# Optimization experiments

Hardware: AMD Instinct MI355X
Metric: run time of the kernel (lower is better)

## Reference

```python
import jax, jax.numpy as jnp
import numpy as np

B, L, C, D, H, NB, K = 8, 1024, 4, 64, 8, 2, 16  # batch, seq, conds, dim, heads, blocks, rbf centers

def _ln(x, s, b):
    m = x.mean(-1, keepdims=True)
    v = x.var(-1, keepdims=True)
    return (x - m) / jnp.sqrt(v + 1e-6) * s + b

def setup_inputs() -> dict:
    key = jax.random.key(0)
    ks = jax.random.split(key, 24)
    rn = lambda i, shape, sc=0.02: jax.random.normal(ks[i], shape, jnp.float32) * sc
    inp = {}
    inp['z'] = jax.random.normal(ks[0], (B, L), jnp.float32)
    inp['conditionals'] = jax.random.normal(ks[1], (C,), jnp.float32)
    inp['s'] = jnp.sort(jax.random.uniform(ks[2], (L,), jnp.float32))
    inp['embed'] = rn(3, (L, 2 * D - (C + 1)))  # positional id embedding table
    # input MLP([4D, D]) with gelu
    inp['Win1'] = rn(4, (2 * D, 4 * D)); inp['bin1'] = jnp.zeros((4 * D,), jnp.float32)
    inp['Win2'] = rn(5, (4 * D, D));     inp['bin2'] = jnp.zeros((D,), jnp.float32)
    # per-block (leading dim NB) transformer params
    inp['ln1_s'] = jnp.ones((NB, D), jnp.float32); inp['ln1_b'] = jnp.zeros((NB, D), jnp.float32)
    inp['ln2_s'] = jnp.ones((NB, D), jnp.float32); inp['ln2_b'] = jnp.zeros((NB, D), jnp.float32)
    inp['Wq'] = rn(6, (NB, D, 2 * D)); inp['bq'] = jnp.zeros((NB, 2 * D), jnp.float32)
    inp['Wk'] = rn(7, (NB, D, 2 * D)); inp['bk'] = jnp.zeros((NB, 2 * D), jnp.float32)
    inp['Wv'] = rn(8, (NB, D, 2 * D)); inp['bv'] = jnp.zeros((NB, 2 * D), jnp.float32)
    inp['Wo'] = rn(9, (NB, 2 * D, D)); inp['bo'] = jnp.zeros((NB, D), jnp.float32)
    # RBF-network attention bias: features exp(-(d-c)^2/(2w^2)) -> linear to H heads
    inp['rbf_c'] = jnp.tile(jnp.linspace(-1.0, 1.0, K, dtype=jnp.float32)[None], (NB, 1))
    inp['rbf_logw'] = jnp.full((NB, K), -1.0, jnp.float32)
    inp['rbf_w'] = rn(10, (NB, K, H), 0.1); inp['rbf_b'] = jnp.zeros((NB, H), jnp.float32)
    # FFN MLP([4D, D])
    inp['W1'] = rn(11, (NB, D, 4 * D)); inp['b1'] = jnp.zeros((NB, 4 * D), jnp.float32)
    inp['W2'] = rn(12, (NB, 4 * D, D)); inp['b2'] = jnp.zeros((NB, D), jnp.float32)
    # head MLP([4D, D, 1])
    inp['Wh1'] = rn(13, (D, 4 * D)); inp['bh1'] = jnp.zeros((4 * D,), jnp.float32)
    inp['Wh2'] = rn(14, (4 * D, D)); inp['bh2'] = jnp.zeros((D,), jnp.float32)
    inp['Wh3'] = rn(15, (D, 1));     inp['bh3'] = jnp.zeros((1,), jnp.float32)
    return inp

def reference(z, conditionals, s, embed, Win1, bin1, Win2, bin2,
              ln1_s, ln1_b, ln2_s, ln2_b, Wq, bq, Wk, bk, Wv, bv, Wo, bo,
              rbf_c, rbf_logw, rbf_w, rbf_b, W1, b1, W2, b2,
              Wh1, bh1, Wh2, bh2, Wh3, bh3):
    Bn, Ln = z.shape
    Cn = conditionals.shape[0]
    Hn = rbf_w.shape[-1]
    dh = Wq.shape[-1] // Hn
    scale = 1.0 / jnp.sqrt(jnp.float32(dh))
    # cond_as_feats: [z, broadcast conditionals] -> (B, L, C+1); prepend ids embedding -> (B, L, 2D)
    feats = jnp.concatenate([
        jnp.broadcast_to(embed[None], (Bn,) + embed.shape),
        z[..., None],
        jnp.broadcast_to(conditionals[None, None, :], (Bn, Ln, Cn)),
    ], axis=-1)
    x = jax.nn.gelu(feats @ Win1 + bin1) @ Win2 + bin2  # (B, L, D)
    dist = s[:, None] - s[None, :]  # (L, L) pairwise query-key coordinate diff (same per batch)
    for i in range(Wq.shape[0]):
        h = _ln(x, ln1_s[i], ln1_b[i])
        q = (h @ Wq[i] + bq[i]).reshape(Bn, Ln, Hn, dh)
        k = (h @ Wk[i] + bk[i]).reshape(Bn, Ln, Hn, dh)
        v = (h @ Wv[i] + bv[i]).reshape(Bn, Ln, Hn, dh)
        scores = jnp.einsum('bqhd,bkhd->bhqk', q, k) * scale
        # RBF-network bias on pairwise distances, per head
        phi = jnp.exp(-(dist[..., None] - rbf_c[i]) ** 2 / (2.0 * jnp.exp(rbf_logw[i]) ** 2))  # (L, L, K)
        bias = jnp.einsum('qkf,fh->hqk', phi, rbf_w[i]) + rbf_b[i][:, None, None]  # (H, L, L)
        a = jax.nn.softmax(scores + bias[None], axis=-1)
        o = jnp.einsum('bhqk,bkhd->bqhd', a, v).reshape(Bn, Ln, Hn * dh)
        x = x + o @ Wo[i] + bo[i]
        h2 = _ln(x, ln2_s[i], ln2_b[i])
        x = x + jax.nn.gelu(h2 @ W1[i] + b1[i]) @ W2[i] + b2[i]
    hh = jax.nn.gelu(x @ Wh1 + bh1)
    hh = jax.nn.gelu(hh @ Wh2 + bh2)
    return hh @ Wh3 + bh3  # f_hat: (B, L, 1)
```

## Files before the change

### kernel.cpp

```cpp
#include <hip/hip_runtime.h>
#include <hip/hip_bf16.h>

#define BB   8
#define LL   1024
#define DD   64
#define D2   128
#define D4   256
#define HH   8
#define DH   16

typedef __attribute__((ext_vector_type(8))) short short8;
typedef __attribute__((ext_vector_type(4))) float floatx4;

#define LOG2E 1.4426950408889634f
#define QK_SEED -66.54214054f

#define OFF_WIN1   0
#define OFF_WIN2   65536
#define OFF_LAY0   98304
#define LAY_STRIDE 131072
#define OFF_WQ     0
#define OFF_WK     16384
#define OFF_WV     32768
#define OFF_WO     49152
#define OFF_W1     65536
#define OFF_W2     98304
#define OFF_WH1    360448
#define OFF_WH2    393216

__device__ __forceinline__ float gelu_tanh(float u) {
  float t = tanhf(0.7978845608028654f * (u + 0.044715f * u * u * u));
  return 0.5f * u * (1.0f + t);
}

__device__ __forceinline__ float wave_reduce_sum(float v) {
#pragma unroll
  for (int m = 32; m >= 1; m >>= 1) v += __shfl_xor(v, m, 64);
  return v;
}

__device__ __forceinline__ unsigned short f2bf(float x) {
  unsigned u = __float_as_uint(x);
  u += 0x7fffu + ((u >> 16) & 1u);
  return (unsigned short)(u >> 16);
}

__device__ __forceinline__ float bf2f(unsigned short x) {
  return __uint_as_float(((unsigned)x) << 16);
}

__device__ __forceinline__ void split_bf(float v, unsigned short& hi,
                                         unsigned short& lo) {
  hi = f2bf(v);
  lo = f2bf(v - bf2f(hi));
}

__device__ __forceinline__ unsigned pack_bf2(float a, float b) {
  unsigned ua = __float_as_uint(a) + 0x8000u;
  unsigned ub = __float_as_uint(b) + 0x8000u;
  return __builtin_amdgcn_perm(ub, ua, 0x07060302u);
}

template <int K, int KP>
__device__ __forceinline__ floatx4 mfma_tile(
    const unsigned short* Ah, const unsigned short* Al,
    const unsigned short* __restrict__ Bh, const unsigned short* __restrict__ Bl,
    int lq, int quad, floatx4 C) {
#pragma unroll
  for (int kk = 0; kk < K; kk += 32) {
    short8 ah = *(const short8*)(Ah + lq * KP + kk + quad * 8);
    short8 al = *(const short8*)(Al + lq * KP + kk + quad * 8);
    short8 bh = *(const short8*)(Bh + lq * K + kk + quad * 8);
    short8 bl = *(const short8*)(Bl + lq * K + kk + quad * 8);
    C = __builtin_amdgcn_mfma_f32_16x16x32_bf16(ah, bh, C, 0, 0, 0);
    C = __builtin_amdgcn_mfma_f32_16x16x32_bf16(al, bh, C, 0, 0, 0);
    C = __builtin_amdgcn_mfma_f32_16x16x32_bf16(ah, bl, C, 0, 0, 0);
  }
  return C;
}

struct PrepArgs {
  const float* src[16];
  int Kd[16], Nd[16], dst[16], elems[16];
};

__global__ __launch_bounds__(256) void k_prep_bias(
    PrepArgs a, unsigned short* __restrict__ arena,
    const float* __restrict__ s, const float* __restrict__ rbf_c,
    const float* __restrict__ rbf_logw, const float* __restrict__ rbf_w,
    const float* __restrict__ rbf_b, unsigned short* __restrict__ biasT) {
  int bid = blockIdx.x, t = threadIdx.x;
  if (bid < 2048) {
    int mid = bid >> 7;
    int e = (bid & 127) * 256 + t;
    int KN = a.elems[mid];
    if (e >= KN) return;
    int K = a.Kd[mid], N = a.Nd[mid];
    int n = e / K, k = e - n * K;
    float wv = a.src[mid][k * N + n];
    unsigned short hi, lo;
    split_bf(wv, hi, lo);
    arena[a.dst[mid] + e] = hi;
    arena[a.dst[mid] + KN + e] = lo;
    return;
  }
  int rem = bid - 2048;
  int lay = rem >> 12;
  int id = (rem & 4095) * 256 + t;
  int q = id >> 10, k = id & 1023;
  float dd = s[q] - s[k];
  float acc[8];
#pragma unroll
  for (int h = 0; h < 8; ++h) acc[h] = rbf_b[lay * 8 + h];
#pragma unroll 1
  for (int f = 0; f < 16; ++f) {
    float c = rbf_c[lay * 16 + f];
    float inv2w2 = 0.5f * __expf(-2.0f * rbf_logw[lay * 16 + f]);
    float e = dd - c;
    float ph = __expf(-e * e * inv2w2);
#pragma unroll
    for (int h = 0; h < 8; ++h)
      acc[h] = fmaf(ph, rbf_w[lay * 128 + f * 8 + h], acc[h]);
  }
  unsigned short* bT = biasT + (size_t)lay * 8 * 1024 * 1024;
#pragma unroll
  for (int h = 0; h < 8; ++h)
    bT[(size_t)(h * 1024 + q) * 1024 + k] = f2bf(acc[h] * LOG2E);
}

__device__ __forceinline__ void qkv_tail(
    const float* xl, unsigned short* Sh, unsigned short* Sl,
    const unsigned short* __restrict__ arena, int lay,
    const float* __restrict__ ln_s, const float* __restrict__ ln_b,
    const float* __restrict__ bq, const float* __restrict__ bk,
    const float* __restrict__ bv, unsigned short* __restrict__ qo,
    unsigned short* __restrict__ ko, unsigned short* __restrict__ voT,
    int tok0, int t) {
  int w = t >> 6, lane = t & 63;
  int lq = lane & 15, quad = lane >> 4;
  float ss = ln_s[lay * 64 + lane], sb = ln_b[lay * 64 + lane];
#pragma unroll
  for (int tk = 0; tk < 4; ++tk) {
    int tok = w * 4 + tk;
    float v = xl[tok * 64 + lane];
    float mean = wave_reduce_sum(v) * 0.015625f;
    float d = v - mean;
    float var = wave_reduce_sum(d * d) * 0.015625f;
    float hv = d * rsqrtf(var + 1e-6f) * ss + sb;
    unsigned short hi, lo;
    split_bf(hv, hi, lo);
    Sh[tok * 72 + lane] = hi;
    Sl[tok * 72 + lane] = lo;
  }
  __syncthreads();
  int b = tok0 >> 10, l0 = tok0 & 1023;
#pragma unroll 1
  for (int mat = 0; mat < 3; ++mat) {
    const unsigned short* Bh =
        arena + OFF_LAY0 + lay * LAY_STRIDE + mat * 16384;
    const unsigned short* Bl = Bh + 8192;
    const float* bias = (mat == 0 ? bq : mat == 1 ? bk : bv) + lay * 128;
#pragma unroll
    for (int j = 0; j < 2; ++j) {
      int tl = w + j * 4;
      int n = tl * 16 + lq;
      float bb = bias[n];
      floatx4 C = {bb, bb, bb, bb};
      C = mfma_tile<64, 72>(Sh, Sl, Bh + tl * 16 * 64, Bl + tl * 16 * 64,
                            lq, quad, C);
      if (mat < 2) {
        unsigned short* outp = (mat == 0 ? qo : ko);
        size_t basea = ((size_t)(b * 8 + tl) * 1024 + l0 + quad * 4) * 16 + lq;
#pragma unroll
        for (int r = 0; r < 4; ++r)
          outp[basea + (size_t)r * 16] = f2bf(C[r]);
      } else {
        size_t basev = ((size_t)(b * 8 + tl) * 16 + lq) * 1024 + l0 + quad * 4;
#pragma unroll
        for (int r = 0; r < 4; ++r)
          voT[basev + r] = f2bf(C[r]);
      }
    }
  }
}

__global__ __launch_bounds__(256) void k_in_qkv(
    const float* __restrict__ embed, const float* __restrict__ z,
    const float* __restrict__ cond, const unsigned short* __restrict__ arena,
    const float* __restrict__ bin1, const float* __restrict__ bin2,
    float* __restrict__ x, const float* __restrict__ ln1_s,
    const float* __restrict__ ln1_b, const float* __restrict__ bq,
    const float* __restrict__ bk, const float* __restrict__ bv,
    unsigned short* __restrict__ qo, unsigned short* __restrict__ ko,
    unsigned short* __restrict__ voT) {
  __shared__ __align__(16) unsigned short Ah[16 * 136], Al[16 * 136];
  __shared__ __align__(16) unsigned short Hh[16 * 264], Hl[16 * 264];
  __shared__ __align__(16) unsigned short Sh[16 * 72], Sl[16 * 72];
  __shared__ float xl[16 * 64];
  int t = threadIdx.x, w = t >> 6, lane = t & 63;
  int lq = lane & 15, quad = lane >> 4;
  int tok0 = blockIdx.x * 16;
  for (int idx = t; idx < 2048; idx += 256) {
    int tok = idx >> 7, dim = idx & 127;
    int bl = tok0 + tok, l = bl & (LL - 1);
    float v;
    if (dim < 123) v = embed[l * 123 + dim];
    else if (dim == 123) v = z[bl];
    else v = cond[dim - 124];
    unsigned short hi, lo;
    split_bf(v, hi, lo);
    Ah[tok * 136 + dim] = hi;
    Al[tok * 136 + dim] = lo;
  }
  __syncthreads();
  const unsigned short* B1h = arena + OFF_WIN1;
  const unsigned short* B1l = B1h + 32768;
#pragma unroll
  for (int j = 0; j < 4; ++j) {
    int tl = w * 4 + j, n = tl * 16 + lq;
    float bb = bin1[n];
    floatx4 C = {bb, bb, bb, bb};
    C = mfma_tile<128, 136>(Ah, Al, B1h + tl * 16 * 128, B1l + tl * 16 * 128,
                            lq, quad, C);
#pragma unroll
    for (int r = 0; r < 4; ++r) {
      float g = gelu_tanh(C[r]);
      unsigned short hi, lo;
      split_bf(g, hi, lo);
      Hh[(quad * 4 + r) * 264 + n] = hi;
      Hl[(quad * 4 + r) * 264 + n] = lo;
    }
  }
  __syncthreads();
  const unsigned short* B2h = arena + OFF_WIN2;
  const unsigned short* B2l = B2h + 16384;
  {
    int n = w * 16 + lq;
    float bb = bin2[n];
    floatx4 C = {bb, bb, bb, bb};
    C = mfma_tile<256, 264>(Hh, Hl, B2h + w * 16 * 256, B2l + w * 16 * 256,
                            lq, quad, C);
#pragma unroll
    for (int r = 0; r < 4; ++r) {
      int m = quad * 4 + r;
      x[(size_t)(tok0 + m) * 64 + n] = C[r];
      xl[m * 64 + n] = C[r];
    }
  }
  __syncthreads();
  qkv_tail(xl, Sh, Sl, arena, 0, ln1_s, ln1_b, bq, bk, bv,
           qo, ko, voT, tok0, t);
}

__global__ __launch_bounds__(256) void k_attn(
    const unsigned short* __restrict__ qg, const unsigned short* __restrict__ kg,
    const unsigned short* __restrict__ vgT, const unsigned short* __restrict__ biasT,
    float* __restrict__ og) {
  __shared__ __align__(16) unsigned short Kl[64 * 32];
  __shared__ __align__(16) unsigned short VT[16 * 72];
  __shared__ __align__(16) unsigned short Pl[4][16 * 72];
  __shared__ __align__(16) unsigned short Bch[64 * 72];
  int t = threadIdx.x, w = t >> 6, lane = t & 63;
  int lq = lane & 15, quad = lane >> 4;
  int bid = blockIdx.x;
  int b = bid >> 7, h = (bid >> 4) & 7, qblk = bid & 15;
  int q0w = qblk * 64 + w * 16;
  size_t bh = (size_t)(b * 8 + h) * 1024;
  size_t bh16 = (size_t)(b * 8 + h) * 16;

  ((uint4*)Kl)[t] = uint4{0, 0, 0, 0};

  short8 Qb = {};
  if (quad < 2)
    Qb = *(const short8*)(qg + (bh + q0w + lq) * 16 + quad * 8);

  float l = 0.0f;
  floatx4 O = {0.0f, 0.0f, 0.0f, 0.0f};

  int key = t >> 2, dp = (t & 3) * 4;
  int drow = t >> 4, vcol = (t & 15) * 4;
  int qrow = t >> 2, bcol = (t & 3) * 16;
  const unsigned short* kgp = kg + (bh + key) * 16 + dp;
  const unsigned short* vgp = vgT + (bh16 + drow) * 1024 + vcol;
  const unsigned short* bgp =
      biasT + ((size_t)(h * 1024 + qblk * 64 + qrow)) * 1024 + bcol;

  uint2 kpre = *(const uint2*)(kgp);
  uint2 vpre = *(const uint2*)(vgp);
  uint4 bpre0 = *(const uint4*)(bgp);
  uint4 bpre1 = *(const uint4*)(bgp + 8);

#pragma unroll 1
  for (int kc = 0; kc < 1024; kc += 64) {
    __syncthreads();
    *(uint2*)(Kl + key * 32 + dp) = kpre;
    *(uint2*)(VT + drow * 72 + vcol) = vpre;
    *(uint4*)(Bch + qrow * 72 + bcol) = bpre0;
    *(uint4*)(Bch + qrow * 72 + bcol + 8) = bpre1;
    __syncthreads();
    if (kc + 64 < 1024) {
      kpre = *(const uint2*)(kgp + (size_t)(kc + 64) * 16);
      vpre = *(const uint2*)(vgp + (kc + 64));
      bpre0 = *(const uint4*)(bgp + (kc + 64));
      bpre1 = *(const uint4*)(bgp + (kc + 64) + 8);
    }
    float psum = 0.0f;
    unsigned short* pw = &Pl[w][lq * 72];
#pragma unroll
    for (int tile = 0; tile < 4; ++tile) {
      short8 A = *(const short8*)(Kl + (tile * 16 + lq) * 32 + quad * 8);
      floatx4 c = {QK_SEED, QK_SEED, QK_SEED, QK_SEED};
      c = __builtin_amdgcn_mfma_f32_16x16x32_bf16(A, Qb, c, 0, 0, 0);
      ushort4 bb = *(const ushort4*)(Bch + (w * 16 + lq) * 72 +
                                     tile * 16 + quad * 4);
      float p0 = exp2f(fmaf(c[0], 0.25f * LOG2E, bf2f(bb.x)));
      float p1 = exp2f(fmaf(c[1], 0.25f * LOG2E, bf2f(bb.y)));
      float p2 = exp2f(fmaf(c[2], 0.25f * LOG2E, bf2f(bb.z)));
      float p3 = exp2f(fmaf(c[3], 0.25f * LOG2E, bf2f(bb.w)));
      psum += (p0 + p1) + (p2 + p3);
      uint2 pk;
      pk.x = pack_bf2(p0, p1);
      pk.y = pack_bf2(p2, p3);
      *(uint2*)(pw + tile * 16 + quad * 4) = pk;
    }
    psum += __shfl_xor(psum, 16, 64);
    psum += __shfl_xor(psum, 32, 64);
    l += psum;
    asm volatile("s_waitcnt lgkmcnt(0)" ::: "memory");
#pragma unroll
    for (int i = 0; i < 2; ++i) {
      short8 Pa = *(const short8*)(pw + i * 32 + quad * 8);
      short8 Vb = *(const short8*)(&VT[lq * 72 + i * 32 + quad * 8]);
      O = __builtin_amdgcn_mfma_f32_16x16x32_bf16(Pa, Vb, O, 0, 0, 0);
    }
  }
  float linv = 1.0f / l;
#pragma unroll
  for (int r = 0; r < 4; ++r) {
    int idx = (quad * 4 + r) * 4;
    float lr = __uint_as_float(
        __builtin_amdgcn_ds_bpermute(idx, __float_as_uint(linv)));
    og[((size_t)(b * 1024 + q0w + quad * 4 + r)) * 128 + h * 16 + lq] = O[r] * lr;
  }
}

__device__ __forceinline__ void pf_body(
    const float* __restrict__ ob, const unsigned short* __restrict__ arena,
    const float* __restrict__ bo, float* __restrict__ x,
    const float* __restrict__ ln_s, const float* __restrict__ ln_b,
    const float* __restrict__ b1, const float* __restrict__ b2, int lay,
    unsigned short* Ah, unsigned short* Al, unsigned short* Sh,
    unsigned short* Sl, unsigned short* Hh, unsigned short* Hl, float* xl,
    int tok0, int t, bool write_x) {
  int w = t >> 6, lane = t & 63;
  int lq = lane & 15, quad = lane >> 4;
  const unsigned short* labase = arena + OFF_LAY0 + lay * LAY_STRIDE;
  for (int idx = t * 4; idx < 2048; idx += 1024) {
    int row = idx >> 7, col = idx & 127;
    float4 v = *(const float4*)(ob + (size_t)(tok0 + row) * 128 + col);
    unsigned short h0, e0, h1, e1, h2, e2, h3, e3;
    split_bf(v.x, h0, e0); split_bf(v.y, h1, e1);
    split_bf(v.z, h2, e2); split_bf(v.w, h3, e3);
    unsigned* ph = (unsigned*)(Ah + row * 136 + col);
    ph[0] = (unsigned)h0 | ((unsigned)h1 << 16);
    ph[1] = (unsigned)h2 | ((unsigned)h3 << 16);
    unsigned* pl = (unsigned*)(Al + row * 136 + col);
    pl[0] = (unsigned)e0 | ((unsigned)e1 << 16);
    pl[1] = (unsigned)e2 | ((unsigned)e3 << 16);
  }
  __syncthreads();
  {
    const unsigned short* Bh = labase + OFF_WO;
    const unsigned short* Bl = Bh + 8192;
    int n = w * 16 + lq;
    float bb = bo[lay * 64 + n];
    floatx4 C = {bb, bb, bb, bb};
    C = mfma_tile<128, 136>(Ah, Al, Bh + w * 16 * 128, Bl + w * 16 * 128,
                            lq, quad, C);
#pragma unroll
    for (int r = 0; r < 4; ++r) {
      int m = quad * 4 + r;
      xl[m * 64 + n] = x[(size_t)(tok0 + m) * 64 + n] + C[r];
    }
  }
  __syncthreads();
  {
    float ss = ln_s[lay * 64 + lane], sb = ln_b[lay * 64 + lane];
#pragma unroll
    for (int tk = 0; tk < 4; ++tk) {
      int tok = w * 4 + tk;
      float v = xl[tok * 64 + lane];
      float mean = wave_reduce_sum(v) * 0.015625f;
      float d = v - mean;
      float var = wave_reduce_sum(d * d) * 0.015625f;
      float hv = d * rsqrtf(var + 1e-6f) * ss + sb;
      unsigned short hi, lo;
      split_bf(hv, hi, lo);
      Sh[tok * 72 + lane] = hi;
      Sl[tok * 72 + lane] = lo;
    }
  }
  __syncthreads();
  {
    const unsigned short* Bh = labase + OFF_W1;
    const unsigned short* Bl = Bh + 16384;
#pragma unroll
    for (int j = 0; j < 4; ++j) {
      int tl = w * 4 + j, n = tl * 16 + lq;
      float bb = b1[lay * 256 + n];
      floatx4 C = {bb, bb, bb, bb};
      C = mfma_tile<64, 72>(Sh, Sl, Bh + tl * 16 * 64, Bl + tl * 16 * 64,
                            lq, quad, C);
#pragma unroll
      for (int r = 0; r < 4; ++r) {
        float g = gelu_tanh(C[r]);
        unsigned short hi, lo;
        split_bf(g, hi, lo);
        Hh[(quad * 4 + r) * 264 + n] = hi;
        Hl[(quad * 4 + r) * 264 + n] = lo;
      }
    }
  }
  __syncthreads();
  {
    const unsigned short* Bh = labase + OFF_W2;
    const unsigned short* Bl = Bh + 16384;
    int n = w * 16 + lq;
    float bb = b2[lay * 64 + n];
    floatx4 C = {bb, bb, bb, bb};
    C = mfma_tile<256, 264>(Hh, Hl, Bh + w * 16 * 256, Bl + w * 16 * 256,
                            lq, quad, C);
#pragma unroll
    for (int r = 0; r < 4; ++r) {
      int m = quad * 4 + r;
      float xv = xl[m * 64 + n] + C[r];
      xl[m * 64 + n] = xv;
      if (write_x) x[(size_t)(tok0 + m) * 64 + n] = xv;
    }
  }
  __syncthreads();
}

__global__ __launch_bounds__(256) void k_pf_qkv(
    const float* __restrict__ ob, const unsigned short* __restrict__ arena,
    const float* __restrict__ bo, float* __restrict__ x,
    const float* __restrict__ ln2_s, const float* __restrict__ ln2_b,
    const float* __restrict__ b1, const float* __restrict__ b2, int lay,
    const float* __restrict__ ln1_s, const float* __restrict__ ln1_b,
    const float* __restrict__ bq, const float* __restrict__ bk,
    const float* __restrict__ bv, unsigned short* __restrict__ qo,
    unsigned short* __restrict__ ko, unsigned short* __restrict__ voT) {
  __shared__ __align__(16) unsigned short Ah[16 * 136], Al[16 * 136];
  __shared__ __align__(16) unsigned short Sh[16 * 72], Sl[16 * 72];
  __shared__ __align__(16) unsigned short Hh[16 * 264], Hl[16 * 264];
  __shared__ float xl[16 * 64];
  int t = threadIdx.x;
  int tok0 = blockIdx.x * 16;
  pf_body(ob, arena, bo, x, ln2_s, ln2_b, b1, b2, lay,
          Ah, Al, Sh, Sl, Hh, Hl, xl, tok0, t, true);
  qkv_tail(xl, Sh, Sl, arena, lay + 1, ln1_s, ln1_b, bq, bk, bv,
           qo, ko, voT, tok0, t);
}

__global__ __launch_bounds__(256) void k_pf_head(
    const float* __restrict__ ob, const unsigned short* __restrict__ arena,
    const float* __restrict__ bo, float* __restrict__ x,
    const float* __restrict__ ln2_s, const float* __restrict__ ln2_b,
    const float* __restrict__ b1, const float* __restrict__ b2, int lay,
    const float* __restrict__ bh1, const float* __restrict__ bh2,
    const float* __restrict__ Wh3, const float* __restrict__ bh3,
    float* __restrict__ out) {
  __shared__ __align__(16) unsigned short Ah[16 * 136], Al[16 * 136];
  __shared__ __align__(16) unsigned short Sh[16 * 72], Sl[16 * 72];
  __shared__ __align__(16) unsigned short Hh[16 * 264], Hl[16 * 264];
  __shared__ float xl[16 * 64];
  int t = threadIdx.x, w = t >> 6, lane = t & 63;
  int lq = lane & 15, quad = lane >> 4;
  int tok0 = blockIdx.x * 16;
  pf_body(ob, arena, bo, x, ln2_s, ln2_b, b1, b2, lay,
          Ah, Al, Sh, Sl, Hh, Hl, xl, tok0, t, false);
#pragma unroll
  for (int tk = 0; tk < 4; ++tk) {
    int tok = w * 4 + tk;
    unsigned short hi, lo;
    split_bf(xl[tok * 64 + lane], hi, lo);
    Sh[tok * 72 + lane] = hi;
    Sl[tok * 72 + lane] = lo;
  }
  __syncthreads();
  {
    const unsigned short* Bh = arena + OFF_WH1;
    const unsigned short* Bl = Bh + 16384;
#pragma unroll
    for (int j = 0; j < 4; ++j) {
      int tl = w * 4 + j, n = tl * 16 + lq;
      float bb = bh1[n];
      floatx4 C = {bb, bb, bb, bb};
      C = mfma_tile<64, 72>(Sh, Sl, Bh + tl * 16 * 64, Bl + tl * 16 * 64,
                            lq, quad, C);
#pragma unroll
      for (int r = 0; r < 4; ++r) {
        float g = gelu_tanh(C[r]);
        unsigned short hi, lo;
        split_bf(g, hi, lo);
        Hh[(quad * 4 + r) * 264 + n] = hi;
        Hl[(quad * 4 + r) * 264 + n] = lo;
      }
    }
  }
  __syncthreads();
  {
    const unsigned short* Bh = arena + OFF_WH2;
    const unsigned short* Bl = Bh + 16384;
    int n = w * 16 + lq;
    float bb = bh2[n];
    floatx4 C = {bb, bb, bb, bb};
    C = mfma_tile<256, 264>(Hh, Hl, Bh + w * 16 * 256, Bl + w * 16 * 256,
                            lq, quad, C);
    __syncthreads();
#pragma unroll
    for (int r = 0; r < 4; ++r)
      xl[(quad * 4 + r) * 64 + n] = gelu_tanh(C[r]);
  }
  __syncthreads();
  float wv3 = Wh3[lane];
#pragma unroll
  for (int tk = 0; tk < 4; ++tk) {
    int tok = w * 4 + tk;
    float v = xl[tok * 64 + lane] * wv3;
    float sum = wave_reduce_sum(v);
    if (lane == 0) out[tok0 + tok] = sum + bh3[0];
  }
}

extern "C" void kernel_launch(void* const* d_in, const int* in_sizes, int n_in,
                              void* d_out, int out_size, void* d_ws, size_t ws_size,
                              hipStream_t stream) {
  const float* z      = (const float*)d_in[0];
  const float* cond   = (const float*)d_in[1];
  const float* s      = (const float*)d_in[2];
  const float* embed  = (const float*)d_in[3];
  const float* Win1   = (const float*)d_in[4];
  const float* bin1   = (const float*)d_in[5];
  const float* Win2   = (const float*)d_in[6];
  const float* bin2   = (const float*)d_in[7];
  const float* ln1_s  = (const float*)d_in[8];
  const float* ln1_b  = (const float*)d_in[9];
  const float* ln2_s  = (const float*)d_in[10];
  const float* ln2_b  = (const float*)d_in[11];
  const float* Wq     = (const float*)d_in[12];
  const float* bq     = (const float*)d_in[13];
  const float* Wk     = (const float*)d_in[14];
  const float* bk     = (const float*)d_in[15];
  const float* Wv     = (const float*)d_in[16];
  const float* bv     = (const float*)d_in[17];
  const float* Wo     = (const float*)d_in[18];
  const float* bo     = (const float*)d_in[19];
  const float* rbf_c  = (const float*)d_in[20];
  const float* rbf_lw = (const float*)d_in[21];
  const float* rbf_w  = (const float*)d_in[22];
  const float* rbf_b  = (const float*)d_in[23];
  const float* W1     = (const float*)d_in[24];
  const float* b1     = (const float*)d_in[25];
  const float* W2     = (const float*)d_in[26];
  const float* b2     = (const float*)d_in[27];
  const float* Wh1    = (const float*)d_in[28];
  const float* bh1    = (const float*)d_in[29];
  const float* Wh2    = (const float*)d_in[30];
  const float* bh2    = (const float*)d_in[31];
  const float* Wh3    = (const float*)d_in[32];
  const float* bh3    = (const float*)d_in[33];

  char* base = (char*)d_ws;
  float*          x     = (float*)(base);
  unsigned short* qb    = (unsigned short*)(base + (2u << 20));
  unsigned short* kb    = (unsigned short*)(base + (4u << 20));
  unsigned short* vbT   = (unsigned short*)(base + (6u << 20));
  float*          ob    = (float*)(base + (8u << 20));
  unsigned short* biasT = (unsigned short*)(base + (12u << 20));
  unsigned short* arena = (unsigned short*)(base + (48u << 20));

  PrepArgs pa;
  auto set = [&](int i, const float* sp, int K, int N, int dst) {
    pa.src[i] = sp; pa.Kd[i] = K; pa.Nd[i] = N; pa.dst[i] = dst;
    pa.elems[i] = K * N;
  };
  set(0, Win1, 128, 256, OFF_WIN1);
  set(1, Win2, 256, 64, OFF_WIN2);
  for (int lay = 0; lay < 2; ++lay) {
    int lb = OFF_LAY0 + lay * LAY_STRIDE;
    set(2 + lay * 6, Wq + lay * 8192, 64, 128, lb + OFF_WQ);
    set(3 + lay * 6, Wk + lay * 8192, 64, 128, lb + OFF_WK);
    set(4 + lay * 6, Wv + lay * 8192, 64, 128, lb + OFF_WV);
    set(5 + lay * 6, Wo + lay * 8192, 128, 64, lb + OFF_WO);
    set(6 + lay * 6, W1 + lay * 16384, 64, 256, lb + OFF_W1);
    set(7 + lay * 6, W2 + lay * 16384, 256, 64, lb + OFF_W2);
  }
  set(14, Wh1, 64, 256, OFF_WH1);
  set(15, Wh2, 256, 64, OFF_WH2);

  k_prep_bias<<<2048 + 8192, 256, 0, stream>>>(pa, arena, s, rbf_c, rbf_lw,
                                               rbf_w, rbf_b, biasT);
  k_in_qkv<<<512, 256, 0, stream>>>(embed, z, cond, arena, bin1, bin2, x,
                                    ln1_s, ln1_b, bq, bk, bv, qb, kb, vbT);
  k_attn<<<1024, 256, 0, stream>>>(qb, kb, vbT, biasT, ob);
  k_pf_qkv<<<512, 256, 0, stream>>>(ob, arena, bo, x, ln2_s, ln2_b, b1, b2, 0,
                                    ln1_s, ln1_b, bq, bk, bv, qb, kb, vbT);
  k_attn<<<1024, 256, 0, stream>>>(qb, kb, vbT,
                                   biasT + (size_t)8 * 1024 * 1024, ob);
  k_pf_head<<<512, 256, 0, stream>>>(ob, arena, bo, x, ln2_s, ln2_b, b1, b2, 1,
                                     bh1, bh2, Wh3, bh3, (float*)d_out);
}
```

Before: 266.4 us.

## Split attention key range in two blocks and merge partial sums downstream

Each attention block now processes only half of the 1024 keys, doubling the grid to 2048 blocks. Each block writes an unnormalized partial output and its row sums to separate buffers. The following post-attention kernels add the two halves and divide by the combined sum. This is meant to raise occupancy and latency hiding in the attention kernel. The cost is an extra fp32 output buffer, more global traffic, and a combine step. The merge is exact only because no running max is kept (a fixed score seed is used instead).

```diff
diff --git a/kernel.cpp b/kernel.cpp
--- a/kernel.cpp
+++ b/kernel.cpp
@@ -14,6 +14,9 @@
 
 #define LOG2E 1.4426950408889634f
 #define QK_SEED -66.54214054f
+
+#define OB_HALF 1048576
+#define L_HALF  65536
 
 #define OFF_WIN1   0
 #define OFF_WIN2   65536
@@ -255,7 +258,7 @@
 __global__ __launch_bounds__(256) void k_attn(
     const unsigned short* __restrict__ qg, const unsigned short* __restrict__ kg,
     const unsigned short* __restrict__ vgT, const unsigned short* __restrict__ biasT,
-    float* __restrict__ og) {
+    float* __restrict__ og, float* __restrict__ lsum) {
   __shared__ __align__(16) unsigned short Kl[64 * 32];
   __shared__ __align__(16) unsigned short VT[16 * 72];
   __shared__ __align__(16) unsigned short Pl[4][16 * 72];
@@ -263,8 +266,11 @@
   int t = threadIdx.x, w = t >> 6, lane = t & 63;
   int lq = lane & 15, quad = lane >> 4;
   int bid = blockIdx.x;
-  int b = bid >> 7, h = (bid >> 4) & 7, qblk = bid & 15;
+  int half = bid >> 10;
+  int rem = bid & 1023;
+  int b = rem >> 7, h = (rem >> 4) & 7, qblk = rem & 15;
   int q0w = qblk * 64 + w * 16;
+  int kbase = half * 512;
   size_t bh = (size_t)(b * 8 + h) * 1024;
   size_t bh16 = (size_t)(b * 8 + h) * 16;
 
@@ -280,10 +286,10 @@
   int key = t >> 2, dp = (t & 3) * 4;
   int drow = t >> 4, vcol = (t & 15) * 4;
   int qrow = t >> 2, bcol = (t & 3) * 16;
-  const unsigned short* kgp = kg + (bh + key) * 16 + dp;
-  const unsigned short* vgp = vgT + (bh16 + drow) * 1024 + vcol;
+  const unsigned short* kgp = kg + (bh + kbase + key) * 16 + dp;
+  const unsigned short* vgp = vgT + (bh16 + drow) * 1024 + kbase + vcol;
   const unsigned short* bgp =
-      biasT + ((size_t)(h * 1024 + qblk * 64 + qrow)) * 1024 + bcol;
+      biasT + ((size_t)(h * 1024 + qblk * 64 + qrow)) * 1024 + kbase + bcol;
 
   uint2 kpre = *(const uint2*)(kgp);
   uint2 vpre = *(const uint2*)(vgp);
@@ -291,14 +297,14 @@
   uint4 bpre1 = *(const uint4*)(bgp + 8);
 
 #pragma unroll 1
-  for (int kc = 0; kc < 1024; kc += 64) {
+  for (int kc = 0; kc < 512; kc += 64) {
     __syncthreads();
     *(uint2*)(Kl + key * 32 + dp) = kpre;
     *(uint2*)(VT + drow * 72 + vcol) = vpre;
     *(uint4*)(Bch + qrow * 72 + bcol) = bpre0;
     *(uint4*)(Bch + qrow * 72 + bcol + 8) = bpre1;
     __syncthreads();
-    if (kc + 64 < 1024) {
+    if (kc + 64 < 512) {
       kpre = *(const uint2*)(kgp + (size_t)(kc + 64) * 16);
       vpre = *(const uint2*)(vgp + (kc + 64));
       bpre0 = *(const uint4*)(bgp + (kc + 64));
@@ -334,18 +340,17 @@
       O = __builtin_amdgcn_mfma_f32_16x16x32_bf16(Pa, Vb, O, 0, 0, 0);
     }
   }
-  float linv = 1.0f / l;
-#pragma unroll
-  for (int r = 0; r < 4; ++r) {
-    int idx = (quad * 4 + r) * 4;
-    float lr = __uint_as_float(
-        __builtin_amdgcn_ds_bpermute(idx, __float_as_uint(linv)));
-    og[((size_t)(b * 1024 + q0w + quad * 4 + r)) * 128 + h * 16 + lq] = O[r] * lr;
-  }
+  float* ogh = og + (size_t)half * OB_HALF;
+#pragma unroll
+  for (int r = 0; r < 4; ++r)
+    ogh[((size_t)(b * 1024 + q0w + quad * 4 + r)) * 128 + h * 16 + lq] = O[r];
+  if (quad == 0)
+    lsum[(size_t)half * L_HALF + (size_t)(b * 1024 + q0w + lq) * 8 + h] = l;
 }
 
 __device__ __forceinline__ void pf_body(
-    const float* __restrict__ ob, const unsigned short* __restrict__ arena,
+    const float* __restrict__ ob, const float* __restrict__ lsum,
+    const unsigned short* __restrict__ arena,
     const float* __restrict__ bo, float* __restrict__ x,
     const float* __restrict__ ln_s, const float* __restrict__ ln_b,
     const float* __restrict__ b1, const float* __restrict__ b2, int lay,
@@ -355,9 +360,21 @@
   int w = t >> 6, lane = t & 63;
   int lq = lane & 15, quad = lane >> 4;
   const unsigned short* labase = arena + OFF_LAY0 + lay * LAY_STRIDE;
+  const float* ob1 = ob + OB_HALF;
   for (int idx = t * 4; idx < 2048; idx += 1024) {
     int row = idx >> 7, col = idx & 127;
-    float4 v = *(const float4*)(ob + (size_t)(tok0 + row) * 128 + col);
+    int hh = col >> 4;
+    int tok = tok0 + row;
+    float lv = lsum[(size_t)tok * 8 + hh] +
+               lsum[L_HALF + (size_t)tok * 8 + hh];
+    float linv = 1.0f / lv;
+    float4 v0 = *(const float4*)(ob + (size_t)tok * 128 + col);
+    float4 v1 = *(const float4*)(ob1 + (size_t)tok * 128 + col);
+    float4 v;
+    v.x = (v0.x + v1.x) * linv;
+    v.y = (v0.y + v1.y) * linv;
+    v.z = (v0.z + v1.z) * linv;
+    v.w = (v0.w + v1.w) * linv;
     unsigned short h0, e0, h1, e1, h2, e2, h3, e3;
     split_bf(v.x, h0, e0); split_bf(v.y, h1, e1);
     split_bf(v.z, h2, e2); split_bf(v.w, h3, e3);
@@ -442,7 +459,8 @@
 }
 
 __global__ __launch_bounds__(256) void k_pf_qkv(
-    const float* __restrict__ ob, const unsigned short* __restrict__ arena,
+    const float* __restrict__ ob, const float* __restrict__ lsum,
+    const unsigned short* __restrict__ arena,
     const float* __restrict__ bo, float* __restrict__ x,
     const float* __restrict__ ln2_s, const float* __restrict__ ln2_b,
     const float* __restrict__ b1, const float* __restrict__ b2, int lay,
@@ -456,14 +474,15 @@
   __shared__ float xl[16 * 64];
   int t = threadIdx.x;
   int tok0 = blockIdx.x * 16;
-  pf_body(ob, arena, bo, x, ln2_s, ln2_b, b1, b2, lay,
+  pf_body(ob, lsum, arena, bo, x, ln2_s, ln2_b, b1, b2, lay,
           Ah, Al, Sh, Sl, Hh, Hl, xl, tok0, t, true);
   qkv_tail(xl, Sh, Sl, arena, lay + 1, ln1_s, ln1_b, bq, bk, bv,
            qo, ko, voT, tok0, t);
 }
 
 __global__ __launch_bounds__(256) void k_pf_head(
-    const float* __restrict__ ob, const unsigned short* __restrict__ arena,
+    const float* __restrict__ ob, const float* __restrict__ lsum,
+    const unsigned short* __restrict__ arena,
     const float* __restrict__ bo, float* __restrict__ x,
     const float* __restrict__ ln2_s, const float* __restrict__ ln2_b,
     const float* __restrict__ b1, const float* __restrict__ b2, int lay,
@@ -477,7 +496,7 @@
   int t = threadIdx.x, w = t >> 6, lane = t & 63;
   int lq = lane & 15, quad = lane >> 4;
   int tok0 = blockIdx.x * 16;
-  pf_body(ob, arena, bo, x, ln2_s, ln2_b, b1, b2, lay,
+  pf_body(ob, lsum, arena, bo, x, ln2_s, ln2_b, b1, b2, lay,
           Ah, Al, Sh, Sl, Hh, Hl, xl, tok0, t, false);
 #pragma unroll
   for (int tk = 0; tk < 4; ++tk) {
@@ -577,8 +596,9 @@
   unsigned short* kb    = (unsigned short*)(base + (4u << 20));
   unsigned short* vbT   = (unsigned short*)(base + (6u << 20));
   float*          ob    = (float*)(base + (8u << 20));
-  unsigned short* biasT = (unsigned short*)(base + (12u << 20));
-  unsigned short* arena = (unsigned short*)(base + (48u << 20));
+  float*          lsum  = (float*)(base + (16u << 20));
+  unsigned short* biasT = (unsigned short*)(base + (17u << 20));
+  unsigned short* arena = (unsigned short*)(base + (50u << 20));
 
   PrepArgs pa;
   auto set = [&](int i, const float* sp, int K, int N, int dst) {
@@ -603,11 +623,13 @@
                                                rbf_w, rbf_b, biasT);
   k_in_qkv<<<512, 256, 0, stream>>>(embed, z, cond, arena, bin1, bin2, x,
                                     ln1_s, ln1_b, bq, bk, bv, qb, kb, vbT);
-  k_attn<<<1024, 256, 0, stream>>>(qb, kb, vbT, biasT, ob);
-  k_pf_qkv<<<512, 256, 0, stream>>>(ob, arena, bo, x, ln2_s, ln2_b, b1, b2, 0,
-                                    ln1_s, ln1_b, bq, bk, bv, qb, kb, vbT);
-  k_attn<<<1024, 256, 0, stream>>>(qb, kb, vbT,
-                                   biasT + (size_t)8 * 1024 * 1024, ob);
-  k_pf_head<<<512, 256, 0, stream>>>(ob, arena, bo, x, ln2_s, ln2_b, b1, b2, 1,
-                                     bh1, bh2, Wh3, bh3, (float*)d_out);
-}
+  k_attn<<<2048, 256, 0, stream>>>(qb, kb, vbT, biasT, ob, lsum);
+  k_pf_qkv<<<512, 256, 0, stream>>>(ob, lsum, arena, bo, x, ln2_s, ln2_b,
+                                    b1, b2, 0, ln1_s, ln1_b, bq, bk, bv,
+                                    qb, kb, vbT);
+  k_attn<<<2048, 256, 0, stream>>>(qb, kb, vbT,
+                                   biasT + (size_t)8 * 1024 * 1024, ob, lsum);
+  k_pf_head<<<512, 256, 0, stream>>>(ob, lsum, arena, bo, x, ln2_s, ln2_b,
+                                     b1, b2, 1, bh1, bh2, Wh3, bh3,
+                                     (float*)d_out);
+}
```

Measured after the change: 264.6 us. No clear change (-0.7%).
